# Optimization experiments

Measured on AMD Instinct MI355X. Metric: run time of the kernel, lower is better.

The kernel has to match this reference:

```python
import jax, jax.numpy as jnp
import numpy as np

B, C_IN, H, W = 8, 256, 32, 32
DK = 256
DV = 256
NH = 8
DKH = DK // NH  # 32
C_OUT = 512
KS, PAD = 3, 1


def setup_inputs() -> dict:
    key = jax.random.key(0)
    ks = jax.random.split(key, 9)
    s = 0.05
    return {
        "x": jax.random.normal(ks[0], (B, C_IN, H, W), jnp.float32),
        "w_qkv": jax.random.normal(ks[1], (2 * DK + DV, C_IN, 1, 1), jnp.float32) * s,
        "b_qkv": jnp.zeros((2 * DK + DV,), jnp.float32),
        "w_attn": jax.random.normal(ks[2], (DV, DV, 1, 1), jnp.float32) * s,
        "b_attn": jnp.zeros((DV,), jnp.float32),
        "w_out": jax.random.normal(ks[3], (C_OUT - DV, C_IN, KS, KS), jnp.float32) * s,
        "b_out": jnp.zeros((C_OUT - DV,), jnp.float32),
        # torch init: dkh**-0.5 + rand
        "key_rel_w": DKH ** (-0.5) + jax.random.uniform(ks[4], (2 * W - 1, DKH), jnp.float32),
        "key_rel_h": DKH ** (-0.5) + jax.random.uniform(ks[5], (2 * H - 1, DKH), jnp.float32),
    }


def conv2d(x, w, b, pad):
    y = jax.lax.conv_general_dilated(
        x, w, window_strides=(1, 1), padding=[(pad, pad), (pad, pad)],
        dimension_numbers=("NCHW", "OIHW", "NCHW"))
    return y + b[None, :, None, None]


def rel_to_abs(x):
    # x: [b, nh, L, 2L-1] -> [b, nh, L, L] (skew trick)
    b, nh, L, _ = x.shape
    x = jnp.pad(x, ((0, 0), (0, 0), (0, 0), (0, 1)))
    flat = x.reshape(b, nh, L * 2 * L)
    flat = jnp.pad(flat, ((0, 0), (0, 0), (0, L - 1)))
    final = flat.reshape(b, nh, L + 1, 2 * L - 1)
    return final[:, :, :L, L - 1:]


def relative_logits_1d(q, rel_k, Hd, Wd, transpose_mask):
    # q: [B, NH, DKH, Hd, Wd]; rel_k: [2*Wd-1, DKH]
    rel = jnp.einsum("bhdxy,md->bhxym", q, rel_k)          # [B,NH,Hd,Wd,2Wd-1]
    rel = rel.reshape(-1, NH * Hd, Wd, 2 * Wd - 1)
    rel = rel_to_abs(rel)                                   # [B,NH*Hd,Wd,Wd]
    rel = rel.reshape(-1, NH, Hd, 1, Wd, Wd)
    rel = jnp.broadcast_to(rel, (rel.shape[0], NH, Hd, Hd, Wd, Wd))
    rel = jnp.transpose(rel, transpose_mask)
    return rel.reshape(-1, NH, Hd * Wd, Hd * Wd)


def reference(x, w_qkv, b_qkv, w_attn, b_attn, w_out, b_out, key_rel_w, key_rel_h):
    conv_out = conv2d(x, w_out, b_out, PAD)                 # [B, C_OUT-DV, H, W]
    qkv = conv2d(x, w_qkv, b_qkv, 0)                        # [B, 2DK+DV, H, W]
    q, k, v = jnp.split(qkv, [DK, 2 * DK], axis=1)
    q = q.reshape(B, NH, DKH, H * W) * (DKH ** -0.5)        # scaled BEFORE rel logits (as in torch)
    k = k.reshape(B, NH, DKH, H * W)
    v = v.reshape(B, NH, DV // NH, H * W)
    logits = jnp.einsum("bhdl,bhdm->bhlm", q, k)            # [B,NH,HW,HW]
    q5 = q.reshape(B, NH, DKH, H, W)
    w_rel = relative_logits_1d(q5, key_rel_w, H, W, (0, 1, 2, 4, 3, 5))
    h_rel = relative_logits_1d(jnp.transpose(q5, (0, 1, 2, 4, 3)), key_rel_h, W, H, (0, 1, 4, 2, 5, 3))
    logits = logits + h_rel + w_rel
    weights = jax.nn.softmax(logits, axis=-1)
    attn = jnp.einsum("bhlm,bhdm->bhdl", weights, v)        # [B,NH,DVH,HW]
    attn = attn.reshape(B, DV, H, W)
    attn = conv2d(attn, w_attn, b_attn, 0)
    return jnp.concatenate([conv_out, attn], axis=1)        # [B, C_OUT, H, W]
```

## Files before the change

kernel.cpp:

```cpp
#include <hip/hip_runtime.h>
#include <hip/hip_bf16.h>


typedef __hip_bfloat16 bf16;
typedef __attribute__((ext_vector_type(8))) short bf16x8;
typedef __attribute__((ext_vector_type(4))) float f32x4;

__device__ __forceinline__ float bf2f(bf16 v) { return __bfloat162float(v); }
__device__ __forceinline__ float blo(unsigned int v) { return __uint_as_float(v << 16); }
__device__ __forceinline__ float bhi(unsigned int v) { return __uint_as_float(v & 0xffff0000u); }
__device__ __forceinline__ unsigned short f2bfbits(float f) {
  union { bf16 h; unsigned short u; } cv; cv.h = __float2bfloat16(f); return cv.u;
}
__device__ __forceinline__ short f2bfr(float f) {
  return (short)((__float_as_uint(f) + 0x8000u) >> 16);
}

__global__ __launch_bounds__(256) void prep_kernel(
    const float* __restrict__ x, const float* __restrict__ wout,
    bf16* __restrict__ xT, bf16* __restrict__ wob0, bf16* __restrict__ wob1)
{
  int bid = blockIdx.x, tid = threadIdx.x;
  if (bid < 2048) {
    __shared__ float t[32 * 33];
    int b = bid >> 8, rem = bid & 255;
    int ci0 = (rem >> 5) * 32, l0 = (rem & 31) * 32;
    {
      int ciL = tid >> 3, lL4 = (tid & 7) * 4;
      float4 v = *(const float4*)(x + (size_t)(b * 256 + ci0 + ciL) * 1024 + l0 + lL4);
      t[ciL * 33 + lL4 + 0] = v.x; t[ciL * 33 + lL4 + 1] = v.y;
      t[ciL * 33 + lL4 + 2] = v.z; t[ciL * 33 + lL4 + 3] = v.w;
    }
    __syncthreads();
    {
      int lL = tid >> 3, cS = (tid & 7) * 4;
      unsigned int p0 = (unsigned int)f2bfbits(t[(cS + 0) * 33 + lL]) |
                        ((unsigned int)f2bfbits(t[(cS + 1) * 33 + lL]) << 16);
      unsigned int p1 = (unsigned int)f2bfbits(t[(cS + 2) * 33 + lL]) |
                        ((unsigned int)f2bfbits(t[(cS + 3) * 33 + lL]) << 16);
      uint2 u2; u2.x = p0; u2.y = p1;
      *(uint2*)(xT + ((size_t)(b * 1024) + l0 + lL) * 256 + ci0 + cS) = u2;
    }
  } else {
    int t0 = (bid - 2048) * 256 + tid;
#pragma unroll
    for (int s = 0; s < 8; ++s) {
      int u = s * 9216 + t0;
      int chunkblk = u / 2304;
      int within = u - chunkblk * 2304;
      int co63 = within / 36;
      int r = within - co63 * 36;
      int kidx = r >> 2, cig = r & 3;
      int co = (chunkblk >> 3) * 64 + co63;
      int ci = (chunkblk & 7) * 32 + cig * 8;
      union { unsigned short h[8]; uint4 u4; } pk;
#pragma unroll
      for (int j = 0; j < 8; ++j)
        pk.h[j] = f2bfbits(wout[(size_t)(co * 256 + ci + j) * 9 + kidx]);
      bf16* dst = (chunkblk < 28) ? (wob0 + (size_t)chunkblk * 18432)
                                  : (wob1 + (size_t)(chunkblk - 28) * 18432);
      *(uint4*)(dst + (size_t)within * 8) = pk.u4;
    }
  }
}

__global__ __launch_bounds__(256) void convqkv_kernel(
    const bf16* __restrict__ xT,
    const bf16* __restrict__ wob0, const bf16* __restrict__ wob1,
    const float* __restrict__ b_out, float* __restrict__ out,
    const float* __restrict__ wq, const float* __restrict__ b_qkv,
    bf16* __restrict__ qT, bf16* __restrict__ kR, bf16* __restrict__ vW)
{
  __shared__ __align__(16) short smem[27104];
  int tid = threadIdx.x, lane = tid & 63, wave = tid >> 6;
  int m16 = lane & 15, quad = lane >> 4;

  if (blockIdx.x < 256) {
    short* wS = smem;
    short* xS = smem + 18944;
    int bid = blockIdx.x;
    int rc = bid & 7, cotile = (bid >> 3) & 3, b = bid >> 5;
    int y0 = rc * 4;

    f32x4 acc[8];
#pragma unroll
    for (int t = 0; t < 8; ++t) acc[t] = (f32x4){0.f, 0.f, 0.f, 0.f};

    for (int ck = 0; ck < 8; ++ck) {
      __syncthreads();
      int cb = cotile * 8 + ck;
      const bf16* wbase = (cb < 28) ? (wob0 + (size_t)cb * 18432)
                                    : (wob1 + (size_t)(cb - 28) * 18432);
#pragma unroll
      for (int r = 0; r < 9; ++r) {
        int u = r * 256 + tid;
        *(uint4*)(wS + (u / 36) * 296 + (u % 36) * 8) = *(const uint4*)(wbase + (size_t)u * 8);
      }
#pragma unroll
      for (int r = 0; r < 3; ++r) {
        int u = r * 256 + tid;
        int pos = u >> 2, seg = u & 3;
        int row = pos >> 5, col = pos & 31;
        int gy = y0 - 1 + row;
        uint4 val = make_uint4(0u, 0u, 0u, 0u);
        if (gy >= 0 && gy < 32)
          val = *(const uint4*)(xT + ((size_t)(b * 1024) + gy * 32 + col) * 256 + ck * 32 + seg * 8);
        *(uint4*)(xS + (row * 34 + col + 1) * 40 + seg * 8) = val;
      }
      if (tid < 48) {
        int pos = tid >> 2, seg = tid & 3;
        int row = pos >> 1, side = pos & 1;
        *(uint4*)(xS + (row * 34 + side * 33) * 40 + seg * 8) = make_uint4(0u, 0u, 0u, 0u);
      }
      __syncthreads();
#pragma unroll
      for (int kidx = 0; kidx < 9; ++kidx) {
        int dy = kidx / 3, dx = kidx - dy * 3;
        bf16x8 af = *(const bf16x8*)(wS + (wave * 16 + m16) * 296 + kidx * 32 + quad * 8);
#pragma unroll
        for (int t = 0; t < 8; ++t) {
          int row = (t >> 1) + dy;
          int col = (t & 1) * 16 + m16 + dx;
          bf16x8 bf = *(const bf16x8*)(xS + (row * 34 + col) * 40 + quad * 8);
          acc[t] = __builtin_amdgcn_mfma_f32_16x16x32_bf16(af, bf, acc[t], 0, 0, 0);
        }
      }
    }

    int cob = cotile * 64 + wave * 16 + quad * 4;
#pragma unroll
    for (int i = 0; i < 4; ++i) {
      float bv = b_out[cob + i];
#pragma unroll
      for (int t = 0; t < 8; ++t) {
        int y = y0 + (t >> 1), xc = (t & 1) * 16 + m16;
        out[((size_t)(b * 512) + cob + i) * 1024 + y * 32 + xc] = acc[t][i] + bv;
      }
    }
  } else {
    short* aS = smem;
    short* bS = smem + 4608;
    int bid2 = blockIdx.x - 256;
    int ltile = bid2 & 7;
    int rest = bid2 >> 3;
    int ctile = rest % 12;
    int b = rest / 12;
    int l0 = ltile * 128;
    int cbase = ctile * 64;

    f32x4 acc[8];
#pragma unroll
    for (int t = 0; t < 8; ++t) acc[t] = (f32x4){0.f, 0.f, 0.f, 0.f};

    for (int ck = 0; ck < 4; ++ck) {
      __syncthreads();
#pragma unroll
      for (int r = 0; r < 4; ++r) {
        int u = r * 256 + tid;
        int c = u >> 4, s4 = u & 15;
        float4 v = *(const float4*)(wq + (size_t)(cbase + c) * 256 + ck * 64 + s4 * 4);
        unsigned int p0 = (unsigned int)f2bfbits(v.x) | ((unsigned int)f2bfbits(v.y) << 16);
        unsigned int p1 = (unsigned int)f2bfbits(v.z) | ((unsigned int)f2bfbits(v.w) << 16);
        uint2 u2; u2.x = p0; u2.y = p1;
        *(uint2*)(aS + c * 72 + s4 * 4) = u2;
      }
#pragma unroll
      for (int r = 0; r < 4; ++r) {
        int u = r * 256 + tid;
        int l = u >> 3, seg = u & 7;
        *(uint4*)(bS + l * 72 + seg * 8) =
            *(const uint4*)(xT + ((size_t)(b * 1024) + l0 + l) * 256 + ck * 64 + seg * 8);
      }
      __syncthreads();
#pragma unroll
      for (int ks = 0; ks < 2; ++ks) {
        bf16x8 af = *(const bf16x8*)(aS + (wave * 16 + m16) * 72 + ks * 32 + quad * 8);
#pragma unroll
        for (int t = 0; t < 8; ++t) {
          bf16x8 bf = *(const bf16x8*)(bS + (t * 16 + m16) * 72 + ks * 32 + quad * 8);
          acc[t] = __builtin_amdgcn_mfma_f32_16x16x32_bf16(af, bf, acc[t], 0, 0, 0);
        }
      }
    }

    __syncthreads();
    short* ldsT = smem + wave * 3072;
    int cb = cbase + wave * 16;
    bool isq = (ctile < 4);
    float bv[4];
#pragma unroll
    for (int i = 0; i < 4; ++i) bv[i] = b_qkv[cb + quad * 4 + i];
#pragma unroll
    for (int t = 0; t < 8; ++t) {
#pragma unroll
      for (int i = 0; i < 4; ++i) {
        float v = acc[t][i] + bv[i];
        if (isq) v *= 0.17677669529663689f;
        ldsT[(t * 16 + m16) * 24 + quad * 4 + i] = (short)f2bfbits(v);
      }
    }
    if (ctile < 8) {
      bf16* dst = isq ? qT : kR;
      int coff = isq ? cb : cb - 256;
#pragma unroll
      for (int rep = 0; rep < 4; ++rep) {
        int u = rep * 64 + lane;
        int l = u >> 1, half = u & 1;
        int c0 = coff + half * 8;
        int head = b * 8 + (c0 >> 5), d0 = c0 & 31;
        *(uint4*)(dst + ((size_t)head * 1024 + l0 + l) * 32 + d0) =
            *(const uint4*)(ldsT + l * 24 + half * 8);
      }
    } else {
      int dcol = lane >> 2, lg = lane & 3;
      int c2 = (cb - 512) + dcol;
      int head = b * 8 + (c2 >> 5), gd = c2 & 31;
#pragma unroll
      for (int s = 0; s < 4; ++s) {
        union { unsigned int w[4]; uint4 u4; } pk;
#pragma unroll
        for (int p = 0; p < 4; ++p) {
          int j0 = lg * 32 + s * 8 + p * 2;
          unsigned int u0 = (unsigned short)ldsT[j0 * 24 + dcol];
          unsigned int u1 = (unsigned short)ldsT[(j0 + 1) * 24 + dcol];
          pk.w[p] = u0 | (u1 << 16);
        }
        *(uint4*)(vW + ((size_t)head * 32 + gd) * 1024 + l0 + lg * 32 + s * 8) = pk.u4;
      }
    }
  }
}

__global__ __launch_bounds__(256) void attn_mfma_kernel(
    const bf16* __restrict__ qT, const bf16* __restrict__ kR, const bf16* __restrict__ vW,
    const float* __restrict__ krw, const float* __restrict__ krh,
    bf16* __restrict__ attL)
{
  __shared__ __align__(16) char smem[27648];
  short* kS   = (short*)smem;
  short* vtS  = (short*)(smem + 5120);
  float* stgF = (float*)smem;
  float* rhS  = (float*)(smem + 9728);
  float* rwS  = (float*)(smem + 18432);

  int tid = threadIdx.x;
  int lane = tid & 63, wave = tid >> 6;
  int m16 = lane & 15, quad = lane >> 4;
  int bid = blockIdx.x;
  int head = ((bid & 7) << 3) | ((bid >> 3) & 7);
  int qt = bid >> 6;
  int row0 = qt * 64;
  int b = head >> 3, h = head & 7;

  int skey = tid >> 2, sseg = tid & 3;
  int svd = tid >> 3, svk = tid & 7;
  const bf16* kptr = kR + (size_t)head * 32768 + skey * 32 + sseg * 8;
  const bf16* vptr = vW + (size_t)head * 32768 + svd * 1024 + svk * 8;
  uint4 kreg = *(const uint4*)kptr;
  uint4 vreg = *(const uint4*)vptr;

  int r = tid >> 2, jseg = tid & 3;
  float q32[32];
  {
    const bf16* qp = qT + ((size_t)head * 1024 + row0 + r) * 32;
#pragma unroll
    for (int s4 = 0; s4 < 4; ++s4) {
      uint4 u = ((const uint4*)qp)[s4];
      q32[s4 * 8 + 0] = blo(u.x); q32[s4 * 8 + 1] = bhi(u.x);
      q32[s4 * 8 + 2] = blo(u.y); q32[s4 * 8 + 3] = bhi(u.y);
      q32[s4 * 8 + 4] = blo(u.z); q32[s4 * 8 + 5] = bhi(u.z);
      q32[s4 * 8 + 6] = blo(u.w); q32[s4 * 8 + 7] = bhi(u.w);
    }
  }

  for (int i = tid; i < 504; i += 256) {
    int row = i >> 3, d0 = (i & 7) * 4;
    *(float4*)(stgF + row * 36 + d0) = *(const float4*)(krw + row * 32 + d0);
  }
  __syncthreads();

  {
    int qi = r & 31;
#pragma unroll
    for (int jj2 = 0; jj2 < 2; ++jj2) {
      float rv[4];
#pragma unroll
      for (int jp = 0; jp < 4; ++jp) {
        int j = jseg * 8 + jj2 * 4 + jp;
        const float* kw = stgF + (j - qi + 31) * 36;
        float s1 = 0.f;
#pragma unroll
        for (int d4 = 0; d4 < 8; ++d4) {
          float4 kv = *(const float4*)(kw + d4 * 4);
          s1 += q32[d4 * 4 + 0] * kv.x + q32[d4 * 4 + 1] * kv.y +
                q32[d4 * 4 + 2] * kv.z + q32[d4 * 4 + 3] * kv.w;
        }
        rv[jp] = s1;
      }
      *(float4*)(rwS + r * 36 + jseg * 8 + jj2 * 4) = make_float4(rv[0], rv[1], rv[2], rv[3]);
    }
  }
  __syncthreads();

  for (int i = tid; i < 504; i += 256) {
    int row = i >> 3, d0 = (i & 7) * 4;
    *(float4*)(stgF + row * 36 + d0) = *(const float4*)(krh + row * 32 + d0);
  }
  __syncthreads();

  {
    int qx = qt * 2 + (r >> 5);
#pragma unroll
    for (int jj = 0; jj < 8; ++jj) {
      int j = jseg * 8 + jj;
      const float* kh = stgF + (j - qx + 31) * 36;
      float s2 = 0.f;
#pragma unroll
      for (int d4 = 0; d4 < 8; ++d4) {
        float4 kv = *(const float4*)(kh + d4 * 4);
        s2 += q32[d4 * 4 + 0] * kv.x + q32[d4 * 4 + 1] * kv.y +
              q32[d4 * 4 + 2] * kv.z + q32[d4 * 4 + 3] * kv.w;
      }
      rhS[j * 68 + r] = s2;
    }
  }
  __syncthreads();

  bf16x8 afrag = *(const bf16x8*)(
      qT + ((size_t)head * 1024 + row0 + wave * 16 + m16) * 32 + quad * 8);
  float rwreg[2][4];
#pragma unroll
  for (int par = 0; par < 2; ++par)
#pragma unroll
    for (int i = 0; i < 4; ++i)
      rwreg[par][i] = rwS[(wave * 16 + quad * 4 + i) * 36 + par * 16 + m16];

  f32x4 oacc[2];
  oacc[0] = (f32x4){0.f, 0.f, 0.f, 0.f};
  oacc[1] = (f32x4){0.f, 0.f, 0.f, 0.f};
  float rsp[4] = {0.f, 0.f, 0.f, 0.f};
  short* pS = (short*)(smem + 18432) + wave * 1152;

  for (int c = 0; c < 16; ++c) {
    __syncthreads();
    *(uint4*)(kS + skey * 40 + sseg * 8) = kreg;
    *(uint4*)(vtS + svd * 72 + svk * 8) = vreg;
    if (c < 15) {
      kreg = *(const uint4*)(kptr + (c + 1) * 2048);
      vreg = *(const uint4*)(vptr + (c + 1) * 64);
    }
    __syncthreads();

    float4 rh0 = *(const float4*)(rhS + (c * 2 + 0) * 68 + wave * 16 + quad * 4);
    float4 rh1 = *(const float4*)(rhS + (c * 2 + 1) * 68 + wave * 16 + quad * 4);
    float rhv[2][4] = {{rh0.x, rh0.y, rh0.z, rh0.w}, {rh1.x, rh1.y, rh1.z, rh1.w}};

    f32x4 sacc[4];
#pragma unroll
    for (int t = 0; t < 4; ++t) {
      bf16x8 bfK = *(const bf16x8*)(kS + (t * 16 + m16) * 40 + quad * 8);
      f32x4 z = (f32x4){0.f, 0.f, 0.f, 0.f};
      sacc[t] = __builtin_amdgcn_mfma_f32_16x16x32_bf16(afrag, bfK, z, 0, 0, 0);
    }
#pragma unroll
    for (int t = 0; t < 4; ++t) {
#pragma unroll
      for (int i = 0; i < 4; ++i) {
        float e = __expf(sacc[t][i] + rwreg[t & 1][i] + rhv[t >> 1][i]);
        rsp[i] += e;
        pS[(quad * 4 + i) * 72 + t * 16 + m16] = f2bfr(e);
      }
    }
#pragma unroll
    for (int ks2 = 0; ks2 < 2; ++ks2) {
      bf16x8 pf = *(const bf16x8*)(pS + m16 * 72 + ks2 * 32 + quad * 8);
#pragma unroll
      for (int dt = 0; dt < 2; ++dt) {
        bf16x8 vf = *(const bf16x8*)(vtS + (dt * 16 + m16) * 72 + ks2 * 32 + quad * 8);
        oacc[dt] = __builtin_amdgcn_mfma_f32_16x16x32_bf16(pf, vf, oacc[dt], 0, 0, 0);
      }
    }
  }

#pragma unroll
  for (int off = 1; off < 16; off <<= 1)
#pragma unroll
    for (int i = 0; i < 4; ++i) rsp[i] += __shfl_xor(rsp[i], off, 64);
#pragma unroll
  for (int i = 0; i < 4; ++i) {
    float invs = 1.0f / rsp[i];
    int grow = row0 + wave * 16 + quad * 4 + i;
#pragma unroll
    for (int dt = 0; dt < 2; ++dt) {
      attL[((size_t)b * 1024 + grow) * 256 + h * 32 + dt * 16 + m16] =
          __float2bfloat16(oacc[dt][i] * invs);
    }
  }
}

__global__ __launch_bounds__(256) void attnout_mfma_kernel(
    const bf16* __restrict__ attL, const float* __restrict__ w, const float* __restrict__ bias,
    float* __restrict__ out)
{
  __shared__ __align__(16) short smem[13824];
  short* aS = smem;
  short* bS = smem + 4608;

  int tid = threadIdx.x, lane = tid & 63, wave = tid >> 6;
  int m16 = lane & 15, quad = lane >> 4;
  int l0 = blockIdx.x * 128;
  int cotile = blockIdx.y;
  int b = blockIdx.z;
  int cbase = cotile * 64;

  f32x4 acc[8];
#pragma unroll
  for (int t = 0; t < 8; ++t) acc[t] = (f32x4){0.f, 0.f, 0.f, 0.f};

  for (int ck = 0; ck < 4; ++ck) {
    __syncthreads();
#pragma unroll
    for (int r = 0; r < 4; ++r) {
      int u = r * 256 + tid;
      int c = u >> 4, s4 = u & 15;
      float4 v = *(const float4*)(w + (size_t)(cbase + c) * 256 + ck * 64 + s4 * 4);
      unsigned int p0 = (unsigned int)f2bfbits(v.x) | ((unsigned int)f2bfbits(v.y) << 16);
      unsigned int p1 = (unsigned int)f2bfbits(v.z) | ((unsigned int)f2bfbits(v.w) << 16);
      uint2 u2; u2.x = p0; u2.y = p1;
      *(uint2*)(aS + c * 72 + s4 * 4) = u2;
    }
#pragma unroll
    for (int r = 0; r < 4; ++r) {
      int u = r * 256 + tid;
      int l = u >> 3, seg = u & 7;
      *(uint4*)(bS + l * 72 + seg * 8) =
          *(const uint4*)(attL + ((size_t)(b * 1024) + l0 + l) * 256 + ck * 64 + seg * 8);
    }
    __syncthreads();
#pragma unroll
    for (int ks = 0; ks < 2; ++ks) {
      bf16x8 af = *(const bf16x8*)(aS + (wave * 16 + m16) * 72 + ks * 32 + quad * 8);
#pragma unroll
      for (int t = 0; t < 8; ++t) {
        bf16x8 bf = *(const bf16x8*)(bS + (t * 16 + m16) * 72 + ks * 32 + quad * 8);
        acc[t] = __builtin_amdgcn_mfma_f32_16x16x32_bf16(af, bf, acc[t], 0, 0, 0);
      }
    }
  }

  int co = cbase + wave * 16 + quad * 4;
#pragma unroll
  for (int i = 0; i < 4; ++i) {
    float bv = bias[co + i];
    size_t obase = ((size_t)(b * 512) + 256 + co + i) * 1024 + l0;
#pragma unroll
    for (int t = 0; t < 8; ++t)
      out[obase + t * 16 + m16] = acc[t][i] + bv;
  }
}

extern "C" void kernel_launch(void* const* d_in, const int* in_sizes, int n_in,
                              void* d_out, int out_size, void* d_ws, size_t ws_size,
                              hipStream_t stream) {
  const float* x      = (const float*)d_in[0];
  const float* w_qkv  = (const float*)d_in[1];
  const float* b_qkv  = (const float*)d_in[2];
  const float* w_attn = (const float*)d_in[3];
  const float* b_attn = (const float*)d_in[4];
  const float* w_out  = (const float*)d_in[5];
  const float* b_out  = (const float*)d_in[6];
  const float* krw    = (const float*)d_in[7];
  const float* krh    = (const float*)d_in[8];
  float* out = (float*)d_out;

  bf16* ws    = (bf16*)d_ws;
  bf16* xT    = ws;
  bf16* attL  = ws;
  bf16* qT    = ws + 2097152;
  bf16* kR    = ws + 4194304;
  bf16* vW    = ws + 6291456;

  bf16* wob0 = (bf16*)(out + (size_t)(0 * 512 + 256) * 1024);
  bf16* wob1 = (bf16*)(out + (size_t)(1 * 512 + 256) * 1024);

  prep_kernel<<<dim3(2084), 256, 0, stream>>>(x, w_out, xT, wob0, wob1);
  convqkv_kernel<<<dim3(1024), 256, 0, stream>>>(xT, wob0, wob1, b_out, out,
                                                 w_qkv, b_qkv, qT, kR, vW);
  attn_mfma_kernel<<<dim3(1024), 256, 0, stream>>>(qT, kR, vW, krw, krh, attL);
  attnout_mfma_kernel<<<dim3(8, 4, 8), 256, 0, stream>>>(attL, w_attn, b_attn, out);
}
```

Baseline: 153.9 us.

## Keep softmax probabilities in registers via transposed MFMA and double-buffer K/V tiles

```diff
diff --git a/kernel.cpp b/kernel.cpp
--- a/kernel.cpp
+++ b/kernel.cpp
@@ -12,8 +12,17 @@
 __device__ __forceinline__ unsigned short f2bfbits(float f) {
   union { bf16 h; unsigned short u; } cv; cv.h = __float2bfloat16(f); return cv.u;
 }
-__device__ __forceinline__ short f2bfr(float f) {
-  return (short)((__float_as_uint(f) + 0x8000u) >> 16);
+__device__ __forceinline__ unsigned int cvt_pk_bf16(float lo, float hi) {
+  unsigned int r;
+  asm("v_cvt_pk_bf16_f32 %0, %1, %2" : "=v"(r) : "v"(lo), "v"(hi));
+  return r;
+}
+__device__ __forceinline__ float exp2_f(float x) {
+#if __has_builtin(__builtin_amdgcn_exp2f)
+  return __builtin_amdgcn_exp2f(x);
+#else
+  return exp2f(x);
+#endif
 }
 
 __global__ __launch_bounds__(256) void prep_kernel(
@@ -236,12 +245,16 @@
     const float* __restrict__ krw, const float* __restrict__ krh,
     bf16* __restrict__ attL)
 {
-  __shared__ __align__(16) char smem[27648];
-  short* kS   = (short*)smem;
-  short* vtS  = (short*)(smem + 5120);
+  __shared__ __align__(16) char smem[37376];
+  short* kS0 = (short*)smem;
+  short* kS1 = (short*)(smem + 5120);
+  short* vt0 = (short*)(smem + 10240);
+  short* vt1 = (short*)(smem + 14848);
   float* stgF = (float*)smem;
-  float* rhS  = (float*)(smem + 9728);
-  float* rwS  = (float*)(smem + 18432);
+  float* rhS  = (float*)(smem + 19456);
+  float* rwS  = (float*)(smem + 28160);
+
+  const float L2E = 1.4426950408889634f;
 
   int tid = threadIdx.x;
   int lane = tid & 63, wave = tid >> 6;
@@ -295,7 +308,7 @@
           s1 += q32[d4 * 4 + 0] * kv.x + q32[d4 * 4 + 1] * kv.y +
                 q32[d4 * 4 + 2] * kv.z + q32[d4 * 4 + 3] * kv.w;
         }
-        rv[jp] = s1;
+        rv[jp] = s1 * L2E;
       }
       *(float4*)(rwS + r * 36 + jseg * 8 + jj2 * 4) = make_float4(rv[0], rv[1], rv[2], rv[3]);
     }
@@ -321,7 +334,7 @@
         s2 += q32[d4 * 4 + 0] * kv.x + q32[d4 * 4 + 1] * kv.y +
               q32[d4 * 4 + 2] * kv.z + q32[d4 * 4 + 3] * kv.w;
       }
-      rhS[j * 68 + r] = s2;
+      rhS[j * 68 + r] = s2 * L2E;
     }
   }
   __syncthreads();
@@ -329,72 +342,89 @@
   bf16x8 afrag = *(const bf16x8*)(
       qT + ((size_t)head * 1024 + row0 + wave * 16 + m16) * 32 + quad * 8);
   float rwreg[2][4];
-#pragma unroll
-  for (int par = 0; par < 2; ++par)
-#pragma unroll
-    for (int i = 0; i < 4; ++i)
-      rwreg[par][i] = rwS[(wave * 16 + quad * 4 + i) * 36 + par * 16 + m16];
+  {
+    float4 rw0 = *(const float4*)(rwS + (wave * 16 + m16) * 36 + quad * 4);
+    float4 rw1 = *(const float4*)(rwS + (wave * 16 + m16) * 36 + 16 + quad * 4);
+    rwreg[0][0] = rw0.x; rwreg[0][1] = rw0.y; rwreg[0][2] = rw0.z; rwreg[0][3] = rw0.w;
+    rwreg[1][0] = rw1.x; rwreg[1][1] = rw1.y; rwreg[1][2] = rw1.z; rwreg[1][3] = rw1.w;
+  }
+
+  *(uint4*)(kS0 + skey * 40 + sseg * 8) = kreg;
+  *(uint4*)(vt0 + svd * 72 + svk * 8) = vreg;
+  kreg = *(const uint4*)(kptr + 2048);
+  vreg = *(const uint4*)(vptr + 64);
 
   f32x4 oacc[2];
   oacc[0] = (f32x4){0.f, 0.f, 0.f, 0.f};
   oacc[1] = (f32x4){0.f, 0.f, 0.f, 0.f};
-  float rsp[4] = {0.f, 0.f, 0.f, 0.f};
-  short* pS = (short*)(smem + 18432) + wave * 1152;
+  float rsp = 0.f;
 
   for (int c = 0; c < 16; ++c) {
     __syncthreads();
-    *(uint4*)(kS + skey * 40 + sseg * 8) = kreg;
-    *(uint4*)(vtS + svd * 72 + svk * 8) = vreg;
     if (c < 15) {
-      kreg = *(const uint4*)(kptr + (c + 1) * 2048);
-      vreg = *(const uint4*)(vptr + (c + 1) * 64);
-    }
-    __syncthreads();
-
-    float4 rh0 = *(const float4*)(rhS + (c * 2 + 0) * 68 + wave * 16 + quad * 4);
-    float4 rh1 = *(const float4*)(rhS + (c * 2 + 1) * 68 + wave * 16 + quad * 4);
-    float rhv[2][4] = {{rh0.x, rh0.y, rh0.z, rh0.w}, {rh1.x, rh1.y, rh1.z, rh1.w}};
+      short* kN = (c & 1) ? kS0 : kS1;
+      short* vN = (c & 1) ? vt0 : vt1;
+      *(uint4*)(kN + skey * 40 + sseg * 8) = kreg;
+      *(uint4*)(vN + svd * 72 + svk * 8) = vreg;
+      if (c < 14) {
+        kreg = *(const uint4*)(kptr + (c + 2) * 2048);
+        vreg = *(const uint4*)(vptr + (c + 2) * 64);
+      }
+    }
+    const short* kC = (c & 1) ? kS1 : kS0;
+    const short* vC = (c & 1) ? vt1 : vt0;
+
+    float rh0 = rhS[(c * 2 + 0) * 68 + wave * 16 + m16];
+    float rh1 = rhS[(c * 2 + 1) * 68 + wave * 16 + m16];
 
     f32x4 sacc[4];
 #pragma unroll
     for (int t = 0; t < 4; ++t) {
-      bf16x8 bfK = *(const bf16x8*)(kS + (t * 16 + m16) * 40 + quad * 8);
+      bf16x8 kf = *(const bf16x8*)(kC + (t * 16 + m16) * 40 + quad * 8);
       f32x4 z = (f32x4){0.f, 0.f, 0.f, 0.f};
-      sacc[t] = __builtin_amdgcn_mfma_f32_16x16x32_bf16(afrag, bfK, z, 0, 0, 0);
-    }
+      sacc[t] = __builtin_amdgcn_mfma_f32_16x16x32_bf16(kf, afrag, z, 0, 0, 0);
+    }
+
+    unsigned int pk[4][2];
 #pragma unroll
     for (int t = 0; t < 4; ++t) {
+      float rh = (t < 2) ? rh0 : rh1;
+      float e[4];
 #pragma unroll
       for (int i = 0; i < 4; ++i) {
-        float e = __expf(sacc[t][i] + rwreg[t & 1][i] + rhv[t >> 1][i]);
-        rsp[i] += e;
-        pS[(quad * 4 + i) * 72 + t * 16 + m16] = f2bfr(e);
-      }
-    }
-#pragma unroll
-    for (int ks2 = 0; ks2 < 2; ++ks2) {
-      bf16x8 pf = *(const bf16x8*)(pS + m16 * 72 + ks2 * 32 + quad * 8);
+        e[i] = exp2_f(fmaf(sacc[t][i], L2E, rwreg[t & 1][i] + rh));
+        rsp += e[i];
+      }
+      pk[t][0] = cvt_pk_bf16(e[0], e[1]);
+      pk[t][1] = cvt_pk_bf16(e[2], e[3]);
+    }
+
+#pragma unroll
+    for (int ks = 0; ks < 2; ++ks) {
+      union { unsigned int w[4]; bf16x8 v; } pf;
+      pf.w[0] = pk[2 * ks][0];     pf.w[1] = pk[2 * ks][1];
+      pf.w[2] = pk[2 * ks + 1][0]; pf.w[3] = pk[2 * ks + 1][1];
 #pragma unroll
       for (int dt = 0; dt < 2; ++dt) {
-        bf16x8 vf = *(const bf16x8*)(vtS + (dt * 16 + m16) * 72 + ks2 * 32 + quad * 8);
-        oacc[dt] = __builtin_amdgcn_mfma_f32_16x16x32_bf16(pf, vf, oacc[dt], 0, 0, 0);
-      }
-    }
-  }
-
-#pragma unroll
-  for (int off = 1; off < 16; off <<= 1)
-#pragma unroll
-    for (int i = 0; i < 4; ++i) rsp[i] += __shfl_xor(rsp[i], off, 64);
-#pragma unroll
-  for (int i = 0; i < 4; ++i) {
-    float invs = 1.0f / rsp[i];
-    int grow = row0 + wave * 16 + quad * 4 + i;
-#pragma unroll
-    for (int dt = 0; dt < 2; ++dt) {
-      attL[((size_t)b * 1024 + grow) * 256 + h * 32 + dt * 16 + m16] =
-          __float2bfloat16(oacc[dt][i] * invs);
-    }
+        const short* vb = vC + (dt * 16 + m16) * 72 + ks * 32 + quad * 4;
+        union { uint2 u[2]; bf16x8 v; } vf;
+        vf.u[0] = *(const uint2*)(vb);
+        vf.u[1] = *(const uint2*)(vb + 16);
+        oacc[dt] = __builtin_amdgcn_mfma_f32_16x16x32_bf16(vf.v, pf.v, oacc[dt], 0, 0, 0);
+      }
+    }
+  }
+
+  rsp += __shfl_xor(rsp, 16, 64);
+  rsp += __shfl_xor(rsp, 32, 64);
+  float invs = 1.0f / rsp;
+  int grow = row0 + wave * 16 + m16;
+#pragma unroll
+  for (int dt = 0; dt < 2; ++dt) {
+    uint2 st;
+    st.x = cvt_pk_bf16(oacc[dt][0] * invs, oacc[dt][1] * invs);
+    st.y = cvt_pk_bf16(oacc[dt][2] * invs, oacc[dt][3] * invs);
+    *(uint2*)(attL + ((size_t)b * 1024 + grow) * 256 + h * 32 + dt * 16 + quad * 4) = st;
   }
 }
 
```

New measurement: 150.0 us. -2.5%, faster.
